# Kernel tuning notes

Hardware: AMD Instinct MI355X
Metric: run time of the kernel (lower is better)

The kernel has to match this reference:

```python
import jax, jax.numpy as jnp
import numpy as np

H = 128; W = 128; HW = H * W
B = 4          # batch_size
D = 256        # feat_dim
HEADS = 8
HD = D // HEADS
S = 256        # num_slots_total
POS = 512      # num_pos_samples
NEG = 256      # num_neg_samples
NS = POS + NEG # num_samples
LN_EPS = 1e-5


def _layer_norm(x, axis=-1, eps=LN_EPS):
    mean = jnp.mean(x, axis=axis, keepdims=True)
    var = jnp.mean(jnp.square(x - mean), axis=axis, keepdims=True)
    return (x - mean) * jax.lax.rsqrt(var + eps)


def setup_inputs() -> dict:
    key = jax.random.key(0)
    ks = jax.random.split(key, 8)
    slots = jax.random.normal(ks[0], (1, S, D), jnp.float32)
    features = jax.random.normal(ks[1], (HW, B, D), jnp.float32)
    pos_encodings = jax.random.normal(ks[2], (HW, B, D), jnp.float32)
    curio_maps = jax.random.uniform(ks[3], (S, H, W), jnp.float32)
    batch_idx = jax.random.randint(ks[4], (S,), 0, B)
    scale = 1.0 / np.sqrt(D)
    in_proj_weight = jax.random.normal(ks[5], (3 * D, D), jnp.float32) * scale
    in_proj_bias = jnp.zeros((3 * D,), jnp.float32)
    out_proj_w = jax.random.normal(ks[6], (D, D), jnp.float32) * scale
    out_proj_b = jnp.zeros((D,), jnp.float32)
    ln_w = jnp.ones((D,), jnp.float32)
    ln_b = jnp.zeros((D,), jnp.float32)
    return {
        'slots': slots, 'features': features, 'pos_encodings': pos_encodings,
        'curio_maps': curio_maps, 'batch_idx': batch_idx,
        'in_proj_weight': in_proj_weight, 'in_proj_bias': in_proj_bias,
        'out_proj_w': out_proj_w, 'out_proj_b': out_proj_b,
        'ln_w': ln_w, 'ln_b': ln_b, 'max_mask_entries': 100,
    }


def reference(slots, features, pos_encodings, curio_maps, batch_idx,
              in_proj_weight, in_proj_bias, out_proj_w, out_proj_b,
              ln_w, ln_b, max_mask_entries):
    ns_total = slots.shape[1]
    # ---- sample(): curiosity-guided top-k sampling -------------------------
    flat = curio_maps.reshape(ns_total, -1)                 # [S, H*W]
    sorted_idx = jnp.argsort(-flat, axis=1)                 # descending
    pos_idx = sorted_idx[:, :POS]
    neg_pool = sorted_idx[:, POS:flat.shape[1] - max_mask_entries]
    # deterministic stand-in for random.sample over the negative pool
    neg_idx = neg_pool[:, :NEG]
    feat_idx = jnp.concatenate([pos_idx, neg_idx], axis=1).T  # [NS, S]

    # ---- update_slots(): gather + projected multi-head cross-attention -----
    bi = batch_idx[None, :]                                 # [1, S]
    f = features[feat_idx, bi, :]                           # [NS, S, D]
    p = pos_encodings[feat_idx, bi, :]                      # [NS, S, D]
    keys = f + p
    values = f[:POS]                                        # [POS, S, D]

    Wq, Wk, Wv = in_proj_weight[:D], in_proj_weight[D:2 * D], in_proj_weight[2 * D:]
    bq, bk, bv = in_proj_bias[:D], in_proj_bias[D:2 * D], in_proj_bias[2 * D:]
    scaling = float(HD) ** -0.5
    q = (jnp.einsum('bsd,ed->bse', slots, Wq) + bq) * scaling   # [1, S, D]
    k = jnp.einsum('nsd,ed->nse', keys, Wk) + bk                # [NS, S, D]
    v = jnp.einsum('nsd,ed->nse', values, Wv) + bv              # [POS, S, D]

    q = q.reshape(ns_total * HEADS, 1, HD)                      # [S*h, 1, hd]
    k = k.reshape(NS, ns_total * HEADS, HD).transpose(1, 0, 2)  # [S*h, NS, hd]
    v = v.reshape(POS, ns_total * HEADS, HD).transpose(1, 0, 2) # [S*h, POS, hd]

    aff = jnp.einsum('nqd,nkd->nqk', q, k)                      # [S*h, 1, NS]
    attn = jax.nn.softmax(aff[:, :, :POS], axis=-1)
    out = jnp.einsum('nqk,nkd->nqd', attn, v)                   # [S*h, 1, hd]
    out = out.reshape(1, ns_total, D)
    out = jnp.einsum('bsd,ed->bse', out, out_proj_w) + out_proj_b

    slots_new = slots + out
    slots_new = _layer_norm(slots_new, axis=-1) * ln_w + ln_b   # [1, S, D]

    # normalized slot-feature affinities (head-averaged, per-slot layernorm)
    aff2 = aff.reshape(ns_total, HEADS, NS).transpose(2, 0, 1)  # [NS, S, h]
    aff2 = jnp.mean(aff2, axis=-1)                              # [NS, S]
    norm_aff = _layer_norm(aff2.T, axis=-1).T                   # [NS, S]
    norm_aff = jax.lax.stop_gradient(norm_aff)
    return slots_new, norm_aff
```

## Files before the change

kernel.cpp:

```cpp
#include <hip/hip_runtime.h>
#include <math.h>

#define NSLOT 256
#define HWN   16384
#define D_    256
#define BB    4
#define NSEL  768
#define NPOS  512
#define NHEAD 8

typedef __attribute__((ext_vector_type(8))) short short8v;
typedef __attribute__((ext_vector_type(4))) float float4v;

#define GLD16(g, l)                                                        \
  __builtin_amdgcn_global_load_lds(                                        \
      (__attribute__((address_space(1))) void*)(g),                        \
      (__attribute__((address_space(3))) void*)(l), 16, 0, 0)

#define BFLO(u) __uint_as_float((u) << 16)
#define BFHI(u) __uint_as_float((u) & 0xffff0000u)

__device__ __forceinline__ unsigned short f2bf(float x) {
  unsigned u = __float_as_uint(x);
  unsigned r = u + 0x7fffu + ((u >> 16) & 1u);
  return (unsigned short)(r >> 16);
}
__device__ __forceinline__ unsigned int pk2(float a, float b) {
  return (unsigned)f2bf(a) | ((unsigned)f2bf(b) << 16);
}

__global__ __launch_bounds__(256) void pack_kernel(const float* __restrict__ f,
                                                   const float* __restrict__ p,
                                                   unsigned short* __restrict__ kpf) {
  int stride = gridDim.x * 256;
  for (int u = blockIdx.x * 256 + threadIdx.x; u < HWN * BB * 32; u += stride) {
    int row = u >> 5, b = u & 31;
    int c8 = b << 3;
    const float4* f4 = (const float4*)(f + (size_t)row * D_ + c8);
    const float4* p4 = (const float4*)(p + (size_t)row * D_ + c8);
    float4 a0 = f4[0], a1 = f4[1], b0 = p4[0], b1 = p4[1];
    uint4 kp, ff;
    kp.x = pk2(a0.x + b0.x, a0.y + b0.y);
    kp.y = pk2(a0.z + b0.z, a0.w + b0.w);
    kp.z = pk2(a1.x + b1.x, a1.y + b1.y);
    kp.w = pk2(a1.z + b1.z, a1.w + b1.w);
    ff.x = pk2(a0.x, a0.y); ff.y = pk2(a0.z, a0.w);
    ff.z = pk2(a1.x, a1.y); ff.w = pk2(a1.z, a1.w);
    int sig = row & 7;
    *(uint4*)(kpf + (size_t)row * 512 + ((b ^ sig) << 3)) = kp;
    *(uint4*)(kpf + (size_t)row * 512 + 256 + (b << 3)) = ff;
  }
}

__global__ __launch_bounds__(1024) void topk_kernel(const float* __restrict__ curio,
                                                    int* __restrict__ feat_sel) {
  __shared__ unsigned int hist[4096];
  __shared__ unsigned int wsum[16];
  __shared__ unsigned long long skey[2048];
  __shared__ int sBstar;
  __shared__ unsigned int sCount;
  int s = blockIdx.x;
  int t = threadIdx.x;
  int wave = t >> 6, lane = t & 63;
  const float* row = curio + (size_t)s * HWN;

  for (int i = t; i < 4096; i += 1024) hist[i] = 0;
  if (t == 0) sCount = 0;
  __syncthreads();
  for (int j = t; j < HWN; j += 1024) {
    unsigned int bits = __float_as_uint(row[j]);
    atomicAdd(&hist[bits >> 18], 1u);
  }
  __syncthreads();
  unsigned int cs = hist[t * 4] + hist[t * 4 + 1] + hist[t * 4 + 2] + hist[t * 4 + 3];
  unsigned int v = cs;
#pragma unroll
  for (int off = 1; off < 64; off <<= 1) {
    unsigned int u = __shfl_down(v, off, 64);
    if (lane + off < 64) v += u;
  }
  if (lane == 0) wsum[wave] = v;
  __syncthreads();
  unsigned int above = 0;
  for (int w2 = wave + 1; w2 < 16; w2++) above += wsum[w2];
  unsigned int sufAfter = above + (v - cs);
  if (sufAfter < NSEL && sufAfter + cs >= NSEL) {
    unsigned int local = sufAfter;
    for (int b = t * 4 + 3; b >= t * 4; b--) {
      unsigned int c = hist[b];
      if (local + c >= NSEL) { sBstar = b; break; }
      local += c;
    }
  }
  __syncthreads();
  int bstar = sBstar;
  for (int j = t; j < HWN; j += 1024) {
    unsigned int bits = __float_as_uint(row[j]);
    if ((int)(bits >> 18) >= bstar) {
      unsigned int pos = atomicAdd(&sCount, 1u);
      if (pos < 2048)
        skey[pos] = ((unsigned long long)bits << 14) | (unsigned long long)(16383 - j);
    }
  }
  __syncthreads();
  unsigned int M = sCount;
  int SZ = (M <= 1024) ? 1024 : 2048;
  for (int i = t; i < SZ; i += 1024) if (i >= (int)M) skey[i] = 0ull;
  for (int k = 2; k <= SZ; k <<= 1) {
    for (int j2 = k >> 1; j2 > 0; j2 >>= 1) {
      __syncthreads();
      for (int i = t; i < SZ; i += 1024) {
        int l = i ^ j2;
        if (l > i) {
          unsigned long long a = skey[i], b = skey[l];
          bool dir = ((i & k) == 0);
          if ((a < b) == dir) { skey[i] = b; skey[l] = a; }
        }
      }
    }
  }
  __syncthreads();
  for (int r = t; r < NSEL; r += 1024)
    feat_sel[s * NSEL + r] = 16383 - (int)(skey[r] & 16383ull);
}

__global__ __launch_bounds__(256) void qproj_kernel(const float* __restrict__ slots,
                                                    const float* __restrict__ ipw,
                                                    const float* __restrict__ ipb,
                                                    float* __restrict__ qk_g,
                                                    float* __restrict__ qbk_g,
                                                    float* __restrict__ qksum_g,
                                                    unsigned short* __restrict__ qkb16) {
  __shared__ float srow[D_];
  __shared__ float qrow[D_];
  __shared__ float qkl[NHEAD][D_];
  __shared__ float qsl[D_];
  int s = blockIdx.x, t = threadIdx.x;
  srow[t] = slots[s * D_ + t];
  __syncthreads();
  {
    const float* wq = ipw + (size_t)t * D_;
    float acc = ipb[t];
    for (int d = 0; d < D_; d++) acc += srow[d] * wq[d];
    qrow[t] = acc * 0.17677669529663689f;
  }
  __syncthreads();
  float qsum = 0.f;
  for (int h = 0; h < NHEAD; h++) {
    const float* wkbase = ipw + (size_t)(D_ + h * 32) * D_ + t;
    float a = 0.f;
    for (int e = 0; e < 32; e++) a += qrow[h * 32 + e] * wkbase[(size_t)e * D_];
    qk_g[((size_t)s * NHEAD + h) * D_ + t] = a;
    qkl[h][t] = a;
    qsum += a;
  }
  qksum_g[s * D_ + t] = qsum;
  qsl[t] = qsum;
  if (t < NHEAD) {
    float a = 0.f;
    for (int e = 0; e < 32; e++) a += qrow[t * 32 + e] * ipb[D_ + t * 32 + e];
    qbk_g[s * NHEAD + t] = a;
  }
  __syncthreads();
  for (int i = 0; i < 16; i++) {
    int e = t * 16 + i;
    int kc = e >> 9, l = (e >> 3) & 63, j = e & 7;
    int cc = l & 15, k = kc * 32 + ((l >> 4) & 3) * 8 + j;
    float v = (cc < NHEAD) ? qkl[cc][k] : ((cc == NHEAD) ? qsl[k] : 0.f);
    qkb16[(size_t)s * 4096 + e] = f2bf(v);
  }
}

__global__ __launch_bounds__(256, 3) void aff_pv_mfma_kernel(
    const unsigned short* __restrict__ kpf,
    const unsigned short* __restrict__ qkb16,
    const int* __restrict__ batch_idx, const int* __restrict__ feat_sel,
    const float* __restrict__ qbk_g,
    float* __restrict__ fbar_part,
    float* __restrict__ expsum_part,
    float* __restrict__ stat_part,
    float* __restrict__ aff2_g) {
  __shared__ unsigned short kplds[4][4096];
  __shared__ unsigned short qkb[4096];
  __shared__ float wlds[4][16][17];
  __shared__ float fbar[NHEAD][D_];
  __shared__ float a2buf[384];
  __shared__ int   sfsel[384];
  __shared__ float esums[4][NHEAD];
  __shared__ float sstat[4][2];
  __shared__ float qbkmean_s;

  int b = blockIdx.x, s = b >> 1, half = b & 1;
  int t = threadIdx.x, w = t >> 6, lane = t & 63;
  int bi = batch_idx[s];
  int col = lane & 15, quad = lane >> 4;

  {
    const uint4* src = (const uint4*)(qkb16 + (size_t)s * 4096);
    ((uint4*)qkb)[t] = src[t];
    ((uint4*)qkb)[t + 256] = src[t + 256];
  }
  for (int i = t; i < 384; i += 256) sfsel[i] = feat_sel[s * NSEL + half + 2 * i];
  for (int i = t; i < NHEAD * D_; i += 256) ((float*)fbar)[i] = 0.f;
  if (t == 0) {
    float m = 0.f;
    for (int h = 0; h < NHEAD; h++) m += qbk_g[s * NHEAD + h];
    qbkmean_s = m * 0.125f;
  }
  __syncthreads();

  unsigned short* kslot = &kplds[w][0];
  float acc[NHEAD][4];
#pragma unroll
  for (int h = 0; h < NHEAD; h++)
#pragma unroll
    for (int c = 0; c < 4; c++) acc[h][c] = 0.f;
  float esum_acc = 0.f;

  auto ISSUE_KP = [&](int L) {
#pragma unroll
    for (int p = 0; p < 8; p++) {
      int r0 = sfsel[L + 2 * p], r1 = sfsel[L + 2 * p + 1];
      unsigned ridx = (unsigned)((lane < 32 ? r0 : r1) * BB + bi);
      const unsigned short* src = kpf + (size_t)ridx * 512 + (lane & 31) * 8;
      GLD16(src, kslot + p * 512);
    }
  };

  ISSUE_KP(w * 64);
#pragma unroll 1
  for (int i = 0; i < 6; i++) {
    int L = (i < 4) ? (w * 64 + i * 16) : (256 + w * 32 + (i - 4) * 16);
    asm volatile("s_waitcnt vmcnt(0)" ::: "memory");
    bool pos = (i < 4);
    uint2 fu[16];
    if (pos) {
#pragma unroll
      for (int r = 0; r < 16; r++)
        fu[r] = *(const uint2*)(kpf + (size_t)((unsigned)sfsel[L + r] * BB + bi) * 512 +
                                256 + lane * 4);
    }
    unsigned sig = ((unsigned)sfsel[L + col] * BB + bi) & 7u;
    short8v afr[8];
#pragma unroll
    for (int kc = 0; kc < 8; kc++) {
      unsigned blk = ((unsigned)(kc * 4 + quad)) ^ sig;
      afr[kc] = *(const short8v*)(kslot + col * 256 + blk * 8);
    }
    asm volatile("s_waitcnt lgkmcnt(0)" ::: "memory");
    __builtin_amdgcn_sched_barrier(0);
    if (i < 5) {
      int Ln = (i < 3) ? (w * 64 + (i + 1) * 16) : (256 + w * 32 + (i - 3) * 16);
      ISSUE_KP(Ln);
    }
    float4v c = {0.f, 0.f, 0.f, 0.f};
#pragma unroll
    for (int kc = 0; kc < 8; kc++) {
      short8v bfr = *(const short8v*)&qkb[(kc * 64 + lane) * 8];
      c = __builtin_amdgcn_mfma_f32_16x16x32_bf16(afr[kc], bfr, c, 0, 0, 0);
    }
    if (pos) {
      if (col < NHEAD) {
        float e0 = __expf(c[0]), e1 = __expf(c[1]), e2 = __expf(c[2]), e3 = __expf(c[3]);
        esum_acc += e0 + e1 + e2 + e3;
        wlds[w][quad * 4 + 0][col] = e0;
        wlds[w][quad * 4 + 1][col] = e1;
        wlds[w][quad * 4 + 2][col] = e2;
        wlds[w][quad * 4 + 3][col] = e3;
      } else if (col == NHEAD) {
        float qm = qbkmean_s;
#pragma unroll
        for (int j = 0; j < 4; j++) a2buf[L + quad * 4 + j] = c[j] * 0.125f + qm;
      }
      asm volatile("s_waitcnt lgkmcnt(0)" ::: "memory");
      __builtin_amdgcn_sched_barrier(0);
#pragma unroll
      for (int r = 0; r < 16; r++) {
        const float4 w0 = *(const float4*)&wlds[w][r][0];
        const float4 w1 = *(const float4*)&wlds[w][r][4];
        float f0 = BFLO(fu[r].x), f1 = BFHI(fu[r].x), f2 = BFLO(fu[r].y), f3 = BFHI(fu[r].y);
        acc[0][0] += w0.x * f0; acc[0][1] += w0.x * f1; acc[0][2] += w0.x * f2; acc[0][3] += w0.x * f3;
        acc[1][0] += w0.y * f0; acc[1][1] += w0.y * f1; acc[1][2] += w0.y * f2; acc[1][3] += w0.y * f3;
        acc[2][0] += w0.z * f0; acc[2][1] += w0.z * f1; acc[2][2] += w0.z * f2; acc[2][3] += w0.z * f3;
        acc[3][0] += w0.w * f0; acc[3][1] += w0.w * f1; acc[3][2] += w0.w * f2; acc[3][3] += w0.w * f3;
        acc[4][0] += w1.x * f0; acc[4][1] += w1.x * f1; acc[4][2] += w1.x * f2; acc[4][3] += w1.x * f3;
        acc[5][0] += w1.y * f0; acc[5][1] += w1.y * f1; acc[5][2] += w1.y * f2; acc[5][3] += w1.y * f3;
        acc[6][0] += w1.z * f0; acc[6][1] += w1.z * f1; acc[6][2] += w1.z * f2; acc[6][3] += w1.z * f3;
        acc[7][0] += w1.w * f0; acc[7][1] += w1.w * f1; acc[7][2] += w1.w * f2; acc[7][3] += w1.w * f3;
      }
    } else {
      if (col == NHEAD) {
        float qm = qbkmean_s;
#pragma unroll
        for (int j = 0; j < 4; j++) a2buf[L + quad * 4 + j] = c[j] * 0.125f + qm;
      }
    }
  }

  esum_acc += __shfl_xor(esum_acc, 16, 64);
  esum_acc += __shfl_xor(esum_acc, 32, 64);
  if (lane < NHEAD) esums[w][lane] = esum_acc;
#pragma unroll
  for (int h = 0; h < NHEAD; h++) {
    atomicAdd(&fbar[h][lane * 4 + 0], acc[h][0]);
    atomicAdd(&fbar[h][lane * 4 + 1], acc[h][1]);
    atomicAdd(&fbar[h][lane * 4 + 2], acc[h][2]);
    atomicAdd(&fbar[h][lane * 4 + 3], acc[h][3]);
  }
  __syncthreads();

  {
    float v1 = a2buf[t];
    float v2 = (t < 128) ? a2buf[256 + t] : 0.f;
    float ls = v1 + v2, lq = v1 * v1 + v2 * v2;
#pragma unroll
    for (int off = 32; off >= 1; off >>= 1) { ls += __shfl_xor(ls, off, 64); lq += __shfl_xor(lq, off, 64); }
    if (lane == 0) { sstat[w][0] = ls; sstat[w][1] = lq; }
  }
  __syncthreads();
  if (t < NHEAD) {
    expsum_part[b * NHEAD + t] = esums[0][t] + esums[1][t] + esums[2][t] + esums[3][t];
  } else if (t == NHEAD) {
    stat_part[b * 2 + 0] = sstat[0][0] + sstat[1][0] + sstat[2][0] + sstat[3][0];
    stat_part[b * 2 + 1] = sstat[0][1] + sstat[1][1] + sstat[2][1] + sstat[3][1];
  }
  aff2_g[s * NSEL + half + 2 * t] = a2buf[t];
  if (t < 128) aff2_g[s * NSEL + half + 2 * (256 + t)] = a2buf[256 + t];
  ((float4*)(fbar_part + (size_t)b * 2048))[t] = ((float4*)fbar)[t];
  ((float4*)(fbar_part + (size_t)b * 2048))[t + 256] = ((float4*)fbar)[t + 256];
}

__global__ __launch_bounds__(1024) void finish_kernel(
    const float* __restrict__ slots,
    const float* __restrict__ expsum_part, const float* __restrict__ stat_part,
    const float* __restrict__ aff2_g, const float* __restrict__ fbar_part,
    const float* __restrict__ ipw, const float* __restrict__ ipb,
    const float* __restrict__ wout, const float* __restrict__ bout,
    const float* __restrict__ lnw, const float* __restrict__ lnb,
    float* __restrict__ slots_new, float* __restrict__ norm_aff) {
  __shared__ float fbar[NHEAD][D_];
  __shared__ float srow[D_];
  __shared__ float outv[D_];
  __shared__ float pq[1024];
  __shared__ float redS[4], redQ[4];
  int s = blockIdx.x, t = threadIdx.x, wave = t >> 6, lane = t & 63;

  float st0 = stat_part[s * 4 + 0] + stat_part[s * 4 + 2];
  float st1 = stat_part[s * 4 + 1] + stat_part[s * 4 + 3];
  float mean_a = st0 * (1.0f / NSEL);
  float var_a = st1 * (1.0f / NSEL) - mean_a * mean_a;
  float rstd_a = rsqrtf(var_a + 1e-5f);
  if (t < NSEL) norm_aff[(size_t)t * NSLOT + s] = (aff2_g[s * NSEL + t] - mean_a) * rstd_a;

  if (t < 512) {
    int h = t >> 6;
    float inv = 1.0f / (expsum_part[s * 16 + h] + expsum_part[s * 16 + 8 + h]);
    const float4 a = ((const float4*)(fbar_part + (size_t)s * 4096))[t];
    const float4 c = ((const float4*)(fbar_part + (size_t)s * 4096 + 2048))[t];
    float4 r;
    r.x = (a.x + c.x) * inv; r.y = (a.y + c.y) * inv;
    r.z = (a.z + c.z) * inv; r.w = (a.w + c.w) * inv;
    ((float4*)fbar)[t] = r;
  }
  if (t < 64) ((float4*)srow)[t] = ((const float4*)(slots + (size_t)s * D_))[t];
  __syncthreads();

  {
    int o = t >> 2, part = t & 3, h = o >> 5;
    const float4* wv = (const float4*)(ipw + (size_t)(2 * D_ + o) * D_ + part * 64);
    float a = 0.f;
#pragma unroll
    for (int i = 0; i < 16; i++) {
      float4 w = wv[i];
      int d = part * 64 + i * 4;
      a += fbar[h][d] * w.x + fbar[h][d + 1] * w.y + fbar[h][d + 2] * w.z + fbar[h][d + 3] * w.w;
    }
    pq[t] = a;
  }
  __syncthreads();
  if (t < D_)
    outv[t] = pq[t * 4] + pq[t * 4 + 1] + pq[t * 4 + 2] + pq[t * 4 + 3] + ipb[2 * D_ + t];
  __syncthreads();

  {
    int o = t >> 2, part = t & 3;
    const float4* w4 = (const float4*)(wout + (size_t)o * D_ + part * 64);
    float a = 0.f;
#pragma unroll
    for (int i = 0; i < 16; i++) {
      float4 w = w4[i];
      int d = part * 64 + i * 4;
      a += outv[d] * w.x + outv[d + 1] * w.y + outv[d + 2] * w.z + outv[d + 3] * w.w;
    }
    pq[t] = a;
  }
  __syncthreads();
  float v = 0.f;
  if (t < D_) {
    v = srow[t] + pq[t * 4] + pq[t * 4 + 1] + pq[t * 4 + 2] + pq[t * 4 + 3] + bout[t];
    float ls = v, lq = v * v;
#pragma unroll
    for (int off = 32; off >= 1; off >>= 1) { ls += __shfl_xor(ls, off, 64); lq += __shfl_xor(lq, off, 64); }
    if (lane == 0) { redS[wave] = ls; redQ[wave] = lq; }
  }
  __syncthreads();
  if (t < D_) {
    float tots = redS[0] + redS[1] + redS[2] + redS[3];
    float totq = redQ[0] + redQ[1] + redQ[2] + redQ[3];
    float mean = tots * (1.0f / D_);
    float var = totq * (1.0f / D_) - mean * mean;
    float rstd = rsqrtf(var + 1e-5f);
    slots_new[s * D_ + t] = (v - mean) * rstd * lnw[t] + lnb[t];
  }
}

extern "C" void kernel_launch(void* const* d_in, const int* in_sizes, int n_in,
                              void* d_out, int out_size, void* d_ws, size_t ws_size,
                              hipStream_t stream) {
  const float* slots    = (const float*)d_in[0];
  const float* features = (const float*)d_in[1];
  const float* posenc   = (const float*)d_in[2];
  const float* curio    = (const float*)d_in[3];
  const int*   batch_idx= (const int*)d_in[4];
  const float* ipw      = (const float*)d_in[5];
  const float* ipb      = (const float*)d_in[6];
  const float* wout     = (const float*)d_in[7];
  const float* bout     = (const float*)d_in[8];
  const float* lnw      = (const float*)d_in[9];
  const float* lnb      = (const float*)d_in[10];

  char* ws = (char*)d_ws;
  size_t off = 0;
  int*   feat_sel    = (int*)(ws + off);   off += 256 * 768 * 4;
  float* qk_g        = (float*)(ws + off); off += 256 * 8 * 256 * 4;
  float* qbk_g       = (float*)(ws + off); off += 256 * 8 * 4;
  float* qksum_g     = (float*)(ws + off); off += 256 * 256 * 4;
  unsigned short* qkb16 = (unsigned short*)(ws + off); off += 256 * 4096 * 2;
  float* fbar_part   = (float*)(ws + off); off += 256 * 2 * 8 * 256 * 4;
  float* expsum_part = (float*)(ws + off); off += 256 * 2 * 8 * 4;
  float* stat_part   = (float*)(ws + off); off += 256 * 2 * 2 * 4;
  float* aff2_g      = (float*)(ws + off); off += 256 * 768 * 4;
  size_t kpf_off = (off + 1023) & ~(size_t)1023;
  unsigned short* kpf = (unsigned short*)(ws + kpf_off);

  float* out_f = (float*)d_out;

  pack_kernel<<<2048, 256, 0, stream>>>(features, posenc, kpf);
  topk_kernel<<<NSLOT, 1024, 0, stream>>>(curio, feat_sel);
  qproj_kernel<<<NSLOT, 256, 0, stream>>>(slots, ipw, ipb, qk_g, qbk_g, qksum_g, qkb16);
  aff_pv_mfma_kernel<<<NSLOT * 2, 256, 0, stream>>>(kpf, qkb16, batch_idx, feat_sel,
                                                    qbk_g, fbar_part, expsum_part,
                                                    stat_part, aff2_g);
  finish_kernel<<<NSLOT, 1024, 0, stream>>>(slots, expsum_part, stat_part, aff2_g,
                                            fbar_part, ipw, ipb, wout, bout, lnw, lnb,
                                            out_f, out_f + 65536);
}
```

Baseline: 161.3 us.

## Merge pack, top-k and query projection into one heterogeneous prep kernel

Combines three independent preprocessing kernels into a single launch that partitions blocks by role: top-k selection, query projection (four slots per block) and feature packing. Launch gaps go away and the memory-bound pack work can overlap with the latency-bound sort and projection work. The now-unused fp32 qk and qksum global writes are also dropped. The cost is that all roles share one 1024-thread block shape and a shared-memory union sized to the largest role, which may lower occupancy for the pack blocks.

```diff
diff --git a/kernel.cpp b/kernel.cpp
--- a/kernel.cpp
+++ b/kernel.cpp
@@ -29,145 +29,154 @@
   return (unsigned)f2bf(a) | ((unsigned)f2bf(b) << 16);
 }
 
-__global__ __launch_bounds__(256) void pack_kernel(const float* __restrict__ f,
-                                                   const float* __restrict__ p,
-                                                   unsigned short* __restrict__ kpf) {
-  int stride = gridDim.x * 256;
-  for (int u = blockIdx.x * 256 + threadIdx.x; u < HWN * BB * 32; u += stride) {
-    int row = u >> 5, b = u & 31;
-    int c8 = b << 3;
-    const float4* f4 = (const float4*)(f + (size_t)row * D_ + c8);
-    const float4* p4 = (const float4*)(p + (size_t)row * D_ + c8);
-    float4 a0 = f4[0], a1 = f4[1], b0 = p4[0], b1 = p4[1];
-    uint4 kp, ff;
-    kp.x = pk2(a0.x + b0.x, a0.y + b0.y);
-    kp.y = pk2(a0.z + b0.z, a0.w + b0.w);
-    kp.z = pk2(a1.x + b1.x, a1.y + b1.y);
-    kp.w = pk2(a1.z + b1.z, a1.w + b1.w);
-    ff.x = pk2(a0.x, a0.y); ff.y = pk2(a0.z, a0.w);
-    ff.z = pk2(a1.x, a1.y); ff.w = pk2(a1.z, a1.w);
-    int sig = row & 7;
-    *(uint4*)(kpf + (size_t)row * 512 + ((b ^ sig) << 3)) = kp;
-    *(uint4*)(kpf + (size_t)row * 512 + 256 + (b << 3)) = ff;
-  }
-}
-
-__global__ __launch_bounds__(1024) void topk_kernel(const float* __restrict__ curio,
-                                                    int* __restrict__ feat_sel) {
-  __shared__ unsigned int hist[4096];
-  __shared__ unsigned int wsum[16];
-  __shared__ unsigned long long skey[2048];
-  __shared__ int sBstar;
-  __shared__ unsigned int sCount;
-  int s = blockIdx.x;
+union PrepSmem {
+  struct {
+    unsigned int hist[4096];
+    unsigned int wsum[16];
+    unsigned long long skey[2048];
+    int sBstar;
+    unsigned int sCount;
+  } tk;
+  struct {
+    float srow[4][D_];
+    float qrow[4][D_];
+    float qkl[4][NHEAD][D_];
+    float qsl[4][D_];
+  } qp;
+};
+
+__global__ __launch_bounds__(1024) void prep_kernel(
+    const float* __restrict__ curio, int* __restrict__ feat_sel,
+    const float* __restrict__ slots, const float* __restrict__ ipw,
+    const float* __restrict__ ipb, float* __restrict__ qbk_g,
+    unsigned short* __restrict__ qkb16,
+    const float* __restrict__ fsrc, const float* __restrict__ psrc,
+    unsigned short* __restrict__ kpf) {
+  __shared__ PrepSmem sm;
+  int B = blockIdx.x;
   int t = threadIdx.x;
-  int wave = t >> 6, lane = t & 63;
-  const float* row = curio + (size_t)s * HWN;
-
-  for (int i = t; i < 4096; i += 1024) hist[i] = 0;
-  if (t == 0) sCount = 0;
-  __syncthreads();
-  for (int j = t; j < HWN; j += 1024) {
-    unsigned int bits = __float_as_uint(row[j]);
-    atomicAdd(&hist[bits >> 18], 1u);
-  }
-  __syncthreads();
-  unsigned int cs = hist[t * 4] + hist[t * 4 + 1] + hist[t * 4 + 2] + hist[t * 4 + 3];
-  unsigned int v = cs;
-#pragma unroll
-  for (int off = 1; off < 64; off <<= 1) {
-    unsigned int u = __shfl_down(v, off, 64);
-    if (lane + off < 64) v += u;
-  }
-  if (lane == 0) wsum[wave] = v;
-  __syncthreads();
-  unsigned int above = 0;
-  for (int w2 = wave + 1; w2 < 16; w2++) above += wsum[w2];
-  unsigned int sufAfter = above + (v - cs);
-  if (sufAfter < NSEL && sufAfter + cs >= NSEL) {
-    unsigned int local = sufAfter;
-    for (int b = t * 4 + 3; b >= t * 4; b--) {
-      unsigned int c = hist[b];
-      if (local + c >= NSEL) { sBstar = b; break; }
-      local += c;
-    }
-  }
-  __syncthreads();
-  int bstar = sBstar;
-  for (int j = t; j < HWN; j += 1024) {
-    unsigned int bits = __float_as_uint(row[j]);
-    if ((int)(bits >> 18) >= bstar) {
-      unsigned int pos = atomicAdd(&sCount, 1u);
-      if (pos < 2048)
-        skey[pos] = ((unsigned long long)bits << 14) | (unsigned long long)(16383 - j);
-    }
-  }
-  __syncthreads();
-  unsigned int M = sCount;
-  int SZ = (M <= 1024) ? 1024 : 2048;
-  for (int i = t; i < SZ; i += 1024) if (i >= (int)M) skey[i] = 0ull;
-  for (int k = 2; k <= SZ; k <<= 1) {
-    for (int j2 = k >> 1; j2 > 0; j2 >>= 1) {
-      __syncthreads();
-      for (int i = t; i < SZ; i += 1024) {
-        int l = i ^ j2;
-        if (l > i) {
-          unsigned long long a = skey[i], b = skey[l];
-          bool dir = ((i & k) == 0);
-          if ((a < b) == dir) { skey[i] = b; skey[l] = a; }
+
+  if (B < 256) {
+    int s = B;
+    int wave = t >> 6, lane = t & 63;
+    const float* row = curio + (size_t)s * HWN;
+
+    for (int i = t; i < 4096; i += 1024) sm.tk.hist[i] = 0;
+    if (t == 0) sm.tk.sCount = 0;
+    __syncthreads();
+    for (int j = t; j < HWN; j += 1024) {
+      unsigned int bits = __float_as_uint(row[j]);
+      atomicAdd(&sm.tk.hist[bits >> 18], 1u);
+    }
+    __syncthreads();
+    unsigned int cs = sm.tk.hist[t * 4] + sm.tk.hist[t * 4 + 1] +
+                      sm.tk.hist[t * 4 + 2] + sm.tk.hist[t * 4 + 3];
+    unsigned int v = cs;
+#pragma unroll
+    for (int off = 1; off < 64; off <<= 1) {
+      unsigned int u = __shfl_down(v, off, 64);
+      if (lane + off < 64) v += u;
+    }
+    if (lane == 0) sm.tk.wsum[wave] = v;
+    __syncthreads();
+    unsigned int above = 0;
+    for (int w2 = wave + 1; w2 < 16; w2++) above += sm.tk.wsum[w2];
+    unsigned int sufAfter = above + (v - cs);
+    if (sufAfter < NSEL && sufAfter + cs >= NSEL) {
+      unsigned int local = sufAfter;
+      for (int b2 = t * 4 + 3; b2 >= t * 4; b2--) {
+        unsigned int c = sm.tk.hist[b2];
+        if (local + c >= NSEL) { sm.tk.sBstar = b2; break; }
+        local += c;
+      }
+    }
+    __syncthreads();
+    int bstar = sm.tk.sBstar;
+    for (int j = t; j < HWN; j += 1024) {
+      unsigned int bits = __float_as_uint(row[j]);
+      if ((int)(bits >> 18) >= bstar) {
+        unsigned int pos = atomicAdd(&sm.tk.sCount, 1u);
+        if (pos < 2048)
+          sm.tk.skey[pos] = ((unsigned long long)bits << 14) |
+                            (unsigned long long)(16383 - j);
+      }
+    }
+    __syncthreads();
+    unsigned int M = sm.tk.sCount;
+    int SZ = (M <= 1024) ? 1024 : 2048;
+    for (int i = t; i < SZ; i += 1024) if (i >= (int)M) sm.tk.skey[i] = 0ull;
+    for (int k = 2; k <= SZ; k <<= 1) {
+      for (int j2 = k >> 1; j2 > 0; j2 >>= 1) {
+        __syncthreads();
+        for (int i = t; i < SZ; i += 1024) {
+          int l = i ^ j2;
+          if (l > i) {
+            unsigned long long a = sm.tk.skey[i], b2 = sm.tk.skey[l];
+            bool dir = ((i & k) == 0);
+            if ((a < b2) == dir) { sm.tk.skey[i] = b2; sm.tk.skey[l] = a; }
+          }
         }
       }
     }
-  }
-  __syncthreads();
-  for (int r = t; r < NSEL; r += 1024)
-    feat_sel[s * NSEL + r] = 16383 - (int)(skey[r] & 16383ull);
-}
-
-__global__ __launch_bounds__(256) void qproj_kernel(const float* __restrict__ slots,
-                                                    const float* __restrict__ ipw,
-                                                    const float* __restrict__ ipb,
-                                                    float* __restrict__ qk_g,
-                                                    float* __restrict__ qbk_g,
-                                                    float* __restrict__ qksum_g,
-                                                    unsigned short* __restrict__ qkb16) {
-  __shared__ float srow[D_];
-  __shared__ float qrow[D_];
-  __shared__ float qkl[NHEAD][D_];
-  __shared__ float qsl[D_];
-  int s = blockIdx.x, t = threadIdx.x;
-  srow[t] = slots[s * D_ + t];
-  __syncthreads();
-  {
-    const float* wq = ipw + (size_t)t * D_;
-    float acc = ipb[t];
-    for (int d = 0; d < D_; d++) acc += srow[d] * wq[d];
-    qrow[t] = acc * 0.17677669529663689f;
-  }
-  __syncthreads();
-  float qsum = 0.f;
-  for (int h = 0; h < NHEAD; h++) {
-    const float* wkbase = ipw + (size_t)(D_ + h * 32) * D_ + t;
-    float a = 0.f;
-    for (int e = 0; e < 32; e++) a += qrow[h * 32 + e] * wkbase[(size_t)e * D_];
-    qk_g[((size_t)s * NHEAD + h) * D_ + t] = a;
-    qkl[h][t] = a;
-    qsum += a;
-  }
-  qksum_g[s * D_ + t] = qsum;
-  qsl[t] = qsum;
-  if (t < NHEAD) {
-    float a = 0.f;
-    for (int e = 0; e < 32; e++) a += qrow[t * 32 + e] * ipb[D_ + t * 32 + e];
-    qbk_g[s * NHEAD + t] = a;
-  }
-  __syncthreads();
-  for (int i = 0; i < 16; i++) {
-    int e = t * 16 + i;
-    int kc = e >> 9, l = (e >> 3) & 63, j = e & 7;
-    int cc = l & 15, k = kc * 32 + ((l >> 4) & 3) * 8 + j;
-    float v = (cc < NHEAD) ? qkl[cc][k] : ((cc == NHEAD) ? qsl[k] : 0.f);
-    qkb16[(size_t)s * 4096 + e] = f2bf(v);
+    __syncthreads();
+    for (int r = t; r < NSEL; r += 1024)
+      feat_sel[s * NSEL + r] = 16383 - (int)(sm.tk.skey[r] & 16383ull);
+  } else if (B < 320) {
+    int sub = t >> 8, tt = t & 255;
+    int s = (B - 256) * 4 + sub;
+    float* srow = sm.qp.srow[sub];
+    float* qrow = sm.qp.qrow[sub];
+    float* qsl = sm.qp.qsl[sub];
+    srow[tt] = slots[s * D_ + tt];
+    __syncthreads();
+    {
+      const float* wq = ipw + (size_t)tt * D_;
+      float acc = ipb[tt];
+      for (int d = 0; d < D_; d++) acc += srow[d] * wq[d];
+      qrow[tt] = acc * 0.17677669529663689f;
+    }
+    __syncthreads();
+    float qsum = 0.f;
+    for (int h = 0; h < NHEAD; h++) {
+      const float* wkbase = ipw + (size_t)(D_ + h * 32) * D_ + tt;
+      float a = 0.f;
+      for (int e = 0; e < 32; e++) a += qrow[h * 32 + e] * wkbase[(size_t)e * D_];
+      sm.qp.qkl[sub][h][tt] = a;
+      qsum += a;
+    }
+    qsl[tt] = qsum;
+    if (tt < NHEAD) {
+      float a = 0.f;
+      for (int e = 0; e < 32; e++) a += qrow[tt * 32 + e] * ipb[D_ + tt * 32 + e];
+      qbk_g[s * NHEAD + tt] = a;
+    }
+    __syncthreads();
+    for (int i = 0; i < 16; i++) {
+      int e = tt * 16 + i;
+      int kc = e >> 9, l = (e >> 3) & 63, j = e & 7;
+      int cc = l & 15, k = kc * 32 + ((l >> 4) & 3) * 8 + j;
+      float v = (cc < NHEAD) ? sm.qp.qkl[sub][cc][k] : ((cc == NHEAD) ? qsl[k] : 0.f);
+      qkb16[(size_t)s * 4096 + e] = f2bf(v);
+    }
+  } else {
+    int stride = 512 * 1024;
+    for (int u = (B - 320) * 1024 + t; u < HWN * BB * 32; u += stride) {
+      int row = u >> 5, b2 = u & 31;
+      int c8 = b2 << 3;
+      const float4* f4 = (const float4*)(fsrc + (size_t)row * D_ + c8);
+      const float4* p4 = (const float4*)(psrc + (size_t)row * D_ + c8);
+      float4 a0 = f4[0], a1 = f4[1], b0 = p4[0], b1 = p4[1];
+      uint4 kp, ff;
+      kp.x = pk2(a0.x + b0.x, a0.y + b0.y);
+      kp.y = pk2(a0.z + b0.z, a0.w + b0.w);
+      kp.z = pk2(a1.x + b1.x, a1.y + b1.y);
+      kp.w = pk2(a1.z + b1.z, a1.w + b1.w);
+      ff.x = pk2(a0.x, a0.y); ff.y = pk2(a0.z, a0.w);
+      ff.z = pk2(a1.x, a1.y); ff.w = pk2(a1.z, a1.w);
+      int sig = row & 7;
+      *(uint4*)(kpf + (size_t)row * 512 + ((b2 ^ sig) << 3)) = kp;
+      *(uint4*)(kpf + (size_t)row * 512 + 256 + (c8)) = ff;
+    }
   }
 }
 
@@ -432,9 +441,7 @@
   char* ws = (char*)d_ws;
   size_t off = 0;
   int*   feat_sel    = (int*)(ws + off);   off += 256 * 768 * 4;
-  float* qk_g        = (float*)(ws + off); off += 256 * 8 * 256 * 4;
   float* qbk_g       = (float*)(ws + off); off += 256 * 8 * 4;
-  float* qksum_g     = (float*)(ws + off); off += 256 * 256 * 4;
   unsigned short* qkb16 = (unsigned short*)(ws + off); off += 256 * 4096 * 2;
   float* fbar_part   = (float*)(ws + off); off += 256 * 2 * 8 * 256 * 4;
   float* expsum_part = (float*)(ws + off); off += 256 * 2 * 8 * 4;
@@ -445,9 +452,8 @@
 
   float* out_f = (float*)d_out;
 
-  pack_kernel<<<2048, 256, 0, stream>>>(features, posenc, kpf);
-  topk_kernel<<<NSLOT, 1024, 0, stream>>>(curio, feat_sel);
-  qproj_kernel<<<NSLOT, 256, 0, stream>>>(slots, ipw, ipb, qk_g, qbk_g, qksum_g, qkb16);
+  prep_kernel<<<832, 1024, 0, stream>>>(curio, feat_sel, slots, ipw, ipb,
+                                        qbk_g, qkb16, features, posenc, kpf);
   aff_pv_mfma_kernel<<<NSLOT * 2, 256, 0, stream>>>(kpf, qkb16, batch_idx, feat_sel,
                                                     qbk_g, fbar_part, expsum_part,
                                                     stat_part, aff2_g);
```

Result: faster. 144.1 us (-10.6%).
